# Kernel optimization log

Hardware: AMD Instinct MI355X
Metric: run time of the kernel (lower is better)

## Reference

```python
import jax, jax.numpy as jnp
import numpy as np

K = 20
NEG = jnp.float32(-1e30)

def _l2norm(x):
    # F.normalize(x, dim=1, p=2) with eps clamp
    n = jnp.sqrt(jnp.sum(x * x, axis=1, keepdims=True))
    return x / jnp.maximum(n, 1e-12)

def setup_inputs() -> dict:
    key = jax.random.key(0)
    k1, k2, k3 = jax.random.split(key, 3)
    h, w, C = 96, 96, 256
    query_label = jax.random.randint(k1, (h, w, 3), 0, 2, dtype=jnp.int64)
    color = jnp.zeros((3,), dtype=jnp.int64)
    q_feat = jax.random.normal(k2, (1, C, h, w), dtype=jnp.float32)
    s_feat = jax.random.normal(k3, (1, C, h, w), dtype=jnp.float32)
    return {"query_label": query_label, "color": color, "q_feat": q_feat, "s_feat": s_feat}

def reference(query_label, color, q_feat, s_feat):
    C = q_feat.shape[1]
    out_hw = s_feat.shape[2:]
    # mask at feature resolution (query_label already sized [h,w,3])
    mask = jnp.all(query_label == color, axis=-1).reshape(-1)      # [M]
    q = q_feat[0].transpose(1, 2, 0).reshape(-1, C)                # [M,C]
    s = s_feat[0].transpose(1, 2, 0).reshape(-1, C)                # [N,C]
    qn = _l2norm(q)
    sn = _l2norm(s)
    sim = sn @ qn.T                                                # [N,M] cosine sims
    # top-K over fg columns == top-K over full row with non-fg masked to -inf
    fg_top = jax.lax.top_k(jnp.where(mask[None, :], sim, NEG), K)[0]
    bg_top = jax.lax.top_k(jnp.where(mask[None, :], NEG, sim), K)[0]
    fg_score = jnp.mean(fg_top, axis=1).reshape(out_hw)
    bg_score = jnp.mean(bg_top, axis=1).reshape(out_hw)
    return fg_score, bg_score
```

## Files before the change

kernel.cpp:

```cpp
#include <hip/hip_runtime.h>
#include <math.h>

#define MTOT 9216
#define CDIM 256
#define KSEL 20
#define NCHUNK 4
#define CHUNKQ 2304
#define BS 32
#define QSTEP 128
#define NSTEP 18
#define NSLAB 72

typedef __attribute__((ext_vector_type(8))) short short8;
typedef __attribute__((ext_vector_type(8))) unsigned short ushort8;
typedef __attribute__((ext_vector_type(4))) float f32x4;
typedef __attribute__((ext_vector_type(2))) _Float16 h2;

__device__ __forceinline__ unsigned short f2bf(float v) {
    unsigned u = __float_as_uint(v);
    u += 0x7FFF + ((u >> 16) & 1);
    return (unsigned short)(u >> 16);
}
__device__ __forceinline__ h2 pkh2(float lo, float hi) {
    auto r = __builtin_amdgcn_cvt_pkrtz(lo, hi);
    h2 h; __builtin_memcpy(&h, &r, 4); return h;
}
__device__ __forceinline__ h2 asH2(unsigned int u) {
    h2 h; __builtin_memcpy(&h, &u, 4); return h;
}
__device__ __forceinline__ unsigned int h2u(h2 h) {
    unsigned int u; __builtin_memcpy(&u, &h, 4); return u;
}
__device__ __forceinline__ h2 h2max(h2 a, h2 b) {
    h2 d; asm("v_pk_max_f16 %0, %1, %2" : "=v"(d) : "v"(a), "v"(b)); return d;
}
__device__ __forceinline__ h2 h2min(h2 a, h2 b) {
    h2 d; asm("v_pk_min_f16 %0, %1, %2" : "=v"(d) : "v"(a), "v"(b)); return d;
}
__device__ __forceinline__ unsigned short hbits(_Float16 x) {
    unsigned short u; __builtin_memcpy(&u, &x, 2); return u;
}
__device__ __forceinline__ float hs2f(unsigned short u) {
    _Float16 x; __builtin_memcpy(&x, &u, 2); return (float)x;
}

__device__ __forceinline__ void ins20p(h2 (&l)[KSEL], h2 v) {
    v = h2max(v, l[0]);
#pragma unroll
    for (int i = 0; i < KSEL - 1; ++i) {
        h2 nxt = l[i + 1];
        l[i] = h2min(nxt, v);
        v = h2max(nxt, v);
    }
    l[KSEL - 1] = v;
}
__device__ __forceinline__ void ins20(float (&l)[KSEL], float v) {
#pragma unroll
    for (int i = 0; i < KSEL - 1; ++i) {
        float nxt = l[i + 1];
        l[i] = fminf(nxt, v);
        v = fmaxf(nxt, v);
    }
    l[KSEL - 1] = v;
}

__global__ __launch_bounds__(256) void prepconv_kernel(
    const int* __restrict__ ql, const int* __restrict__ color,
    const float* __restrict__ qf, const float* __restrict__ sf,
    int* __restrict__ cnt,
    unsigned short* __restrict__ qbt, unsigned short* __restrict__ sbt)
{
    __shared__ float tilef[32 * 257];
    __shared__ float red[256];
    __shared__ float invv[32];
    __shared__ int slotl[32];
    const int bid = blockIdx.x;
    const bool isQ = bid < (MTOT / 32);
    const int m0 = (isQ ? bid : bid - MTOT / 32) * 32;
    const float* src = isQ ? qf : sf;
    const int t = threadIdx.x;
    const int ml = t & 31, cb = t >> 5;
    float sq = 0.f;
#pragma unroll
    for (int i = 0; i < 32; ++i) {
        int c = cb * 32 + i;
        float v = src[c * MTOT + m0 + ml];
        tilef[ml * 257 + c] = v;
        sq += v * v;
    }
    red[cb * 32 + ml] = sq;
    __syncthreads();
    if (t < 32) {
        float s = 0.f;
#pragma unroll
        for (int j = 0; j < 8; ++j) s += red[j * 32 + t];
        invv[t] = 1.0f / fmaxf(sqrtf(s), 1e-12f);
        if (isQ) {
            int m = m0 + t;
            bool fg = (ql[3*m] == color[0]) & (ql[3*m+1] == color[1]) & (ql[3*m+2] == color[2]);
            slotl[t] = fg ? atomicAdd(&cnt[0], 1) : (MTOT - 1 - atomicAdd(&cnt[1], 1));
        }
    }
    __syncthreads();
    const int row = t >> 3, seg = t & 7;
    const float iv = invv[row];
    const int drow = isQ ? slotl[row] : (m0 + row);
    unsigned short* dst = (isQ ? qbt : sbt) + (size_t)drow * 256 + seg * 32;
    const float* srcr = &tilef[row * 257 + seg * 32];
#pragma unroll
    for (int ch = 0; ch < 4; ++ch) {
        ushort8 o;
#pragma unroll
        for (int e = 0; e < 8; ++e) o[e] = f2bf(srcr[ch * 8 + e] * iv);
        *(ushort8*)(dst + ch * 8) = o;
    }
}

__global__ __launch_bounds__(256, 3) void matchsim_kernel(
    const unsigned short* __restrict__ qbt, const unsigned short* __restrict__ sbt,
    const int* __restrict__ cnt, unsigned short* __restrict__ part)
{
    __shared__ __align__(16) char smem[49152];
    unsigned int* mbuf = (unsigned int*)smem;

    const int t = threadIdx.x;
    const int w = t >> 6, l = t & 63;
    const int sblk = blockIdx.x >> 2;
    const int chunk = blockIdx.x & 3;
    const int s0 = sblk * BS;
    const int q0c = chunk * CHUNKQ;
    const int fgc = cnt[0];

    {
        int row = t >> 3, cb = t & 7;
        const ushort8* gs = (const ushort8*)(sbt + (size_t)(s0 + row) * 256);
#pragma unroll
        for (int i = 0; i < 4; ++i) {
            int ch = cb + i * 8;
            ushort8 v = gs[ch];
            int byte = (row * 512 + ch * 16) ^ ((row & 7) << 4);
            *(ushort8*)(smem + byte) = v;
        }
    }
    __syncthreads();

    const h2 NEG2 = { (_Float16)-65504.f, (_Float16)-65504.f };
    h2 fgl[KSEL], bgl[KSEL];
#pragma unroll
    for (int i = 0; i < KSEL; ++i) { fgl[i] = NEG2; bgl[i] = NEG2; }

    ushort8 qr[4];
    const int wl = (t & 63) >> 1;
    const int qhalf = t & 1;
    auto loadQ = [&](int gslab) {
        int step = gslab >> 2, slab = gslab & 3;
        const unsigned short* base =
            qbt + (size_t)(q0c + step * QSTEP + w * 32 + wl) * 256 + slab * 64 + qhalf * 32;
#pragma unroll
        for (int i = 0; i < 4; ++i)
            qr[i] = *(const ushort8*)(base + i * 8);
    };
    loadQ(0);
    const int qwswz = (wl & 7) << 4;
    char* const qbase = smem + 16384 + w * 4096;

    const int lg = l >> 4;
    const int aq0 = l & 15;
    const int aq1 = aq0 + 16;
    const int aswz0 = (aq0 & 7) << 4, aswz1 = (aq1 & 7) << 4;
    const int srow0 = l & 15, srow1 = srow0 + 16;
    const int bswz0 = (srow0 & 7) << 4, bswz1 = (srow1 & 7) << 4;

    f32x4 acc00 = {0,0,0,0}, acc01 = {0,0,0,0}, acc10 = {0,0,0,0}, acc11 = {0,0,0,0};
    int cur = 0;

    for (int gslab = 0; gslab < NSLAB; ++gslab) {
        char* Qs = qbase + cur * 16384;
#pragma unroll
        for (int i = 0; i < 4; ++i) {
            int byte = (wl * 128 + qhalf * 64 + i * 16) ^ qwswz;
            *(ushort8*)(Qs + byte) = qr[i];
        }
        if (gslab + 1 < NSLAB) loadQ(gslab + 1);
        const int slab = gslab & 3;
        __builtin_amdgcn_s_setprio(1);
#pragma unroll
        for (int ks = 0; ks < 2; ++ks) {
            int ak = ks * 64 + lg * 16;
            short8 a0 = *(const short8*)(Qs + ((aq0 * 128 + ak) ^ aswz0));
            short8 a1 = *(const short8*)(Qs + ((aq1 * 128 + ak) ^ aswz1));
            int bk = slab * 128 + ks * 64 + lg * 16;
            short8 b0 = *(const short8*)(smem + ((srow0 * 512 + bk) ^ bswz0));
            short8 b1 = *(const short8*)(smem + ((srow1 * 512 + bk) ^ bswz1));
            acc00 = __builtin_amdgcn_mfma_f32_16x16x32_bf16(a0, b0, acc00, 0, 0, 0);
            acc01 = __builtin_amdgcn_mfma_f32_16x16x32_bf16(a0, b1, acc01, 0, 0, 0);
            acc10 = __builtin_amdgcn_mfma_f32_16x16x32_bf16(a1, b0, acc10, 0, 0, 0);
            acc11 = __builtin_amdgcn_mfma_f32_16x16x32_bf16(a1, b1, acc11, 0, 0, 0);
        }
        __builtin_amdgcn_s_setprio(0);
        cur ^= 1;
        if (slab == 3) {
            const int step = gslab >> 2;
            const int qw0 = q0c + step * QSTEP + w * 32;
#pragma unroll
            for (int qt = 0; qt < 2; ++qt) {
                const f32x4& aS0 = qt ? acc10 : acc00;
                const f32x4& aS1 = qt ? acc11 : acc01;
                int qfirst = qw0 + qt * 16;
                if (qfirst + 16 <= fgc) {
#pragma unroll
                    for (int r = 0; r < 4; ++r) ins20p(fgl, pkh2(aS0[r], aS1[r]));
                } else if (qfirst >= fgc) {
#pragma unroll
                    for (int r = 0; r < 4; ++r) ins20p(bgl, pkh2(aS0[r], aS1[r]));
                } else {
#pragma unroll
                    for (int r = 0; r < 4; ++r) {
                        h2 v = pkh2(aS0[r], aS1[r]);
                        bool m = (qfirst + lg * 4 + r) < fgc;
                        ins20p(fgl, m ? v : NEG2);
                        ins20p(bgl, m ? NEG2 : v);
                    }
                }
            }
            acc00 = (f32x4){0,0,0,0}; acc01 = (f32x4){0,0,0,0};
            acc10 = (f32x4){0,0,0,0}; acc11 = (f32x4){0,0,0,0};
        }
    }

    __syncthreads();
    const int sp = l & 15, owner = w * 4 + lg;
    auto midx = [](int cls, int own, int spi) { return ((cls * 16 + own) * 16 + spi) * 21; };
    {
        unsigned int* df = &mbuf[midx(0, owner, sp)];
        unsigned int* db = &mbuf[midx(1, owner, sp)];
#pragma unroll
        for (int k = 0; k < KSEL; ++k) { df[k] = h2u(fgl[k]); db[k] = h2u(bgl[k]); }
    }
    __syncthreads();
    auto mergeL = [&](unsigned int* A, const unsigned int* B) {
        h2 la[KSEL];
#pragma unroll
        for (int k = 0; k < KSEL; ++k) la[k] = asH2(A[k]);
        for (int j = KSEL - 1; j >= 0; --j) {
            h2 v = asH2(B[j]);
            if (!(v.x > la[0].x || v.y > la[0].y)) break;
            ins20p(la, v);
        }
#pragma unroll
        for (int k = 0; k < KSEL; ++k) A[k] = h2u(la[k]);
    };
    {
        int cls = t >> 7, u = t & 127, spi = u & 15, j = u >> 4;
        mergeL(&mbuf[midx(cls, j, spi)], &mbuf[midx(cls, j + 8, spi)]);
    }
    __syncthreads();
    if (t < 128) {
        int cls = t >> 6, u = t & 63, spi = u & 15, j = u >> 4;
        mergeL(&mbuf[midx(cls, j, spi)], &mbuf[midx(cls, j + 4, spi)]);
    }
    __syncthreads();
    if (t < 64) {
        int cls = t >> 5, u = t & 31, spi = u & 15, j = u >> 4;
        mergeL(&mbuf[midx(cls, j, spi)], &mbuf[midx(cls, j + 2, spi)]);
    }
    __syncthreads();
    if (t < 32) {
        int cls = t >> 4, spi = t & 15;
        unsigned int* A = &mbuf[midx(cls, 0, spi)];
        const unsigned int* B = &mbuf[midx(cls, 1, spi)];
        h2 la[KSEL];
#pragma unroll
        for (int k = 0; k < KSEL; ++k) la[k] = asH2(A[k]);
        for (int j = KSEL - 1; j >= 0; --j) {
            h2 v = asH2(B[j]);
            if (!(v.x > la[0].x || v.y > la[0].y)) break;
            ins20p(la, v);
        }
        unsigned short* d0 = &part[((size_t)(s0 + spi)      * NCHUNK + chunk) * (2*KSEL) + cls*KSEL];
        unsigned short* d1 = &part[((size_t)(s0 + 16 + spi) * NCHUNK + chunk) * (2*KSEL) + cls*KSEL];
#pragma unroll
        for (int k = 0; k < KSEL; ++k) {
            d0[k] = hbits(la[k].x);
            d1[k] = hbits(la[k].y);
        }
    }
}

__global__ __launch_bounds__(256) void finalize_kernel(
    const unsigned short* __restrict__ part, float* __restrict__ out)
{
    int n = blockIdx.x * 256 + threadIdx.x;
    if (n >= MTOT) return;
    const unsigned short* base = part + (size_t)n * NCHUNK * 2 * KSEL;
#pragma unroll
    for (int cls = 0; cls < 2; ++cls) {
        float la[KSEL];
        const unsigned short* c0p = base + cls * KSEL;
#pragma unroll
        for (int k = 0; k < KSEL; ++k) la[k] = hs2f(c0p[k]);
        for (int ch = 1; ch < NCHUNK; ++ch) {
            const unsigned short* sp = base + ch * 2 * KSEL + cls * KSEL;
            for (int j = KSEL - 1; j >= 0; --j) {
                float v = hs2f(sp[j]);
                if (v <= la[0]) break;
                ins20(la, v);
            }
        }
        float s = 0.f;
#pragma unroll
        for (int k = 0; k < KSEL; ++k) s += la[k];
        out[cls * MTOT + n] = s * (1.0f / KSEL);
    }
}

extern "C" void kernel_launch(void* const* d_in, const int* in_sizes, int n_in,
                              void* d_out, int out_size, void* d_ws, size_t ws_size,
                              hipStream_t stream) {
    const int*   ql    = (const int*)d_in[0];
    const int*   color = (const int*)d_in[1];
    const float* qf    = (const float*)d_in[2];
    const float* sf    = (const float*)d_in[3];
    float* out = (float*)d_out;

    int* cnt = (int*)d_ws;
    unsigned short* qbt = (unsigned short*)(cnt + 4);
    unsigned short* sbt = qbt + (size_t)MTOT * CDIM;
    unsigned short* part = sbt + (size_t)MTOT * CDIM;

    (void)hipMemsetAsync(cnt, 0, 16, stream);
    prepconv_kernel<<<2 * (MTOT / 32), 256, 0, stream>>>(ql, color, qf, sf, cnt, qbt, sbt);
    matchsim_kernel<<<(MTOT / BS) * NCHUNK, 256, 0, stream>>>(qbt, sbt, cnt, part);
    finalize_kernel<<<MTOT / 256, 256, 0, stream>>>(part, out);
}
```

Baseline: 183.1 us.

## Cache support B fragments in registers and split query range into eight chunks

```diff
diff --git a/kernel.cpp b/kernel.cpp
--- a/kernel.cpp
+++ b/kernel.cpp
@@ -4,12 +4,12 @@
 #define MTOT 9216
 #define CDIM 256
 #define KSEL 20
-#define NCHUNK 4
-#define CHUNKQ 2304
+#define NCHUNK 8
+#define CHUNKQ 1152
 #define BS 32
 #define QSTEP 128
-#define NSTEP 18
-#define NSLAB 72
+#define NSTEP 9
+#define NSLAB 36
 
 typedef __attribute__((ext_vector_type(8))) short short8;
 typedef __attribute__((ext_vector_type(8))) unsigned short ushort8;
@@ -125,8 +125,8 @@
 
     const int t = threadIdx.x;
     const int w = t >> 6, l = t & 63;
-    const int sblk = blockIdx.x >> 2;
-    const int chunk = blockIdx.x & 3;
+    const int sblk = blockIdx.x >> 3;
+    const int chunk = blockIdx.x & 7;
     const int s0 = sblk * BS;
     const int q0c = chunk * CHUNKQ;
     const int fgc = cnt[0];
@@ -144,14 +144,31 @@
     }
     __syncthreads();
 
+    const int lg = l >> 4;
+    const int aq0 = l & 15;
+    const int aq1 = aq0 + 16;
+    const int aswz0 = (aq0 & 7) << 4, aswz1 = (aq1 & 7) << 4;
+    const int srow0 = l & 15, srow1 = srow0 + 16;
+    const int bswz0 = (srow0 & 7) << 4, bswz1 = (srow1 & 7) << 4;
+
+    short8 Bf[16];
+#pragma unroll
+    for (int sl = 0; sl < 4; ++sl)
+#pragma unroll
+        for (int ks = 0; ks < 2; ++ks) {
+            int bk = sl * 128 + ks * 64 + lg * 16;
+            Bf[sl * 4 + ks * 2 + 0] = *(const short8*)(smem + ((srow0 * 512 + bk) ^ bswz0));
+            Bf[sl * 4 + ks * 2 + 1] = *(const short8*)(smem + ((srow1 * 512 + bk) ^ bswz1));
+        }
+
     const h2 NEG2 = { (_Float16)-65504.f, (_Float16)-65504.f };
     h2 fgl[KSEL], bgl[KSEL];
 #pragma unroll
     for (int i = 0; i < KSEL; ++i) { fgl[i] = NEG2; bgl[i] = NEG2; }
 
-    ushort8 qr[4];
     const int wl = (t & 63) >> 1;
     const int qhalf = t & 1;
+    ushort8 qr[4];
     auto loadQ = [&](int gslab) {
         int step = gslab >> 2, slab = gslab & 3;
         const unsigned short* base =
@@ -164,68 +181,56 @@
     const int qwswz = (wl & 7) << 4;
     char* const qbase = smem + 16384 + w * 4096;
 
-    const int lg = l >> 4;
-    const int aq0 = l & 15;
-    const int aq1 = aq0 + 16;
-    const int aswz0 = (aq0 & 7) << 4, aswz1 = (aq1 & 7) << 4;
-    const int srow0 = l & 15, srow1 = srow0 + 16;
-    const int bswz0 = (srow0 & 7) << 4, bswz1 = (srow1 & 7) << 4;
-
     f32x4 acc00 = {0,0,0,0}, acc01 = {0,0,0,0}, acc10 = {0,0,0,0}, acc11 = {0,0,0,0};
-    int cur = 0;
-
-    for (int gslab = 0; gslab < NSLAB; ++gslab) {
-        char* Qs = qbase + cur * 16384;
-#pragma unroll
-        for (int i = 0; i < 4; ++i) {
-            int byte = (wl * 128 + qhalf * 64 + i * 16) ^ qwswz;
-            *(ushort8*)(Qs + byte) = qr[i];
-        }
-        if (gslab + 1 < NSLAB) loadQ(gslab + 1);
-        const int slab = gslab & 3;
-        __builtin_amdgcn_s_setprio(1);
-#pragma unroll
-        for (int ks = 0; ks < 2; ++ks) {
-            int ak = ks * 64 + lg * 16;
-            short8 a0 = *(const short8*)(Qs + ((aq0 * 128 + ak) ^ aswz0));
-            short8 a1 = *(const short8*)(Qs + ((aq1 * 128 + ak) ^ aswz1));
-            int bk = slab * 128 + ks * 64 + lg * 16;
-            short8 b0 = *(const short8*)(smem + ((srow0 * 512 + bk) ^ bswz0));
-            short8 b1 = *(const short8*)(smem + ((srow1 * 512 + bk) ^ bswz1));
-            acc00 = __builtin_amdgcn_mfma_f32_16x16x32_bf16(a0, b0, acc00, 0, 0, 0);
-            acc01 = __builtin_amdgcn_mfma_f32_16x16x32_bf16(a0, b1, acc01, 0, 0, 0);
-            acc10 = __builtin_amdgcn_mfma_f32_16x16x32_bf16(a1, b0, acc10, 0, 0, 0);
-            acc11 = __builtin_amdgcn_mfma_f32_16x16x32_bf16(a1, b1, acc11, 0, 0, 0);
-        }
-        __builtin_amdgcn_s_setprio(0);
-        cur ^= 1;
-        if (slab == 3) {
-            const int step = gslab >> 2;
-            const int qw0 = q0c + step * QSTEP + w * 32;
-#pragma unroll
-            for (int qt = 0; qt < 2; ++qt) {
-                const f32x4& aS0 = qt ? acc10 : acc00;
-                const f32x4& aS1 = qt ? acc11 : acc01;
-                int qfirst = qw0 + qt * 16;
-                if (qfirst + 16 <= fgc) {
-#pragma unroll
-                    for (int r = 0; r < 4; ++r) ins20p(fgl, pkh2(aS0[r], aS1[r]));
-                } else if (qfirst >= fgc) {
-#pragma unroll
-                    for (int r = 0; r < 4; ++r) ins20p(bgl, pkh2(aS0[r], aS1[r]));
-                } else {
-#pragma unroll
-                    for (int r = 0; r < 4; ++r) {
-                        h2 v = pkh2(aS0[r], aS1[r]);
-                        bool m = (qfirst + lg * 4 + r) < fgc;
-                        ins20p(fgl, m ? v : NEG2);
-                        ins20p(bgl, m ? NEG2 : v);
-                    }
+
+    for (int step = 0; step < NSTEP; ++step) {
+#pragma unroll
+        for (int sl = 0; sl < 4; ++sl) {
+            const int gslab = step * 4 + sl;
+            char* Qs = qbase + (sl & 1) * 16384;
+#pragma unroll
+            for (int i = 0; i < 4; ++i) {
+                int byte = (wl * 128 + qhalf * 64 + i * 16) ^ qwswz;
+                *(ushort8*)(Qs + byte) = qr[i];
+            }
+            if (gslab + 1 < NSLAB) loadQ(gslab + 1);
+            __builtin_amdgcn_s_setprio(1);
+#pragma unroll
+            for (int ks = 0; ks < 2; ++ks) {
+                int ak = ks * 64 + lg * 16;
+                short8 a0 = *(const short8*)(Qs + ((aq0 * 128 + ak) ^ aswz0));
+                short8 a1 = *(const short8*)(Qs + ((aq1 * 128 + ak) ^ aswz1));
+                acc00 = __builtin_amdgcn_mfma_f32_16x16x32_bf16(a0, Bf[sl*4+ks*2+0], acc00, 0, 0, 0);
+                acc01 = __builtin_amdgcn_mfma_f32_16x16x32_bf16(a0, Bf[sl*4+ks*2+1], acc01, 0, 0, 0);
+                acc10 = __builtin_amdgcn_mfma_f32_16x16x32_bf16(a1, Bf[sl*4+ks*2+0], acc10, 0, 0, 0);
+                acc11 = __builtin_amdgcn_mfma_f32_16x16x32_bf16(a1, Bf[sl*4+ks*2+1], acc11, 0, 0, 0);
+            }
+            __builtin_amdgcn_s_setprio(0);
+        }
+        const int qw0 = q0c + step * QSTEP + w * 32;
+#pragma unroll
+        for (int qt = 0; qt < 2; ++qt) {
+            const f32x4& aS0 = qt ? acc10 : acc00;
+            const f32x4& aS1 = qt ? acc11 : acc01;
+            int qfirst = qw0 + qt * 16;
+            if (qfirst + 16 <= fgc) {
+#pragma unroll
+                for (int r = 0; r < 4; ++r) ins20p(fgl, pkh2(aS0[r], aS1[r]));
+            } else if (qfirst >= fgc) {
+#pragma unroll
+                for (int r = 0; r < 4; ++r) ins20p(bgl, pkh2(aS0[r], aS1[r]));
+            } else {
+#pragma unroll
+                for (int r = 0; r < 4; ++r) {
+                    h2 v = pkh2(aS0[r], aS1[r]);
+                    bool m = (qfirst + lg * 4 + r) < fgc;
+                    ins20p(fgl, m ? v : NEG2);
+                    ins20p(bgl, m ? NEG2 : v);
                 }
             }
-            acc00 = (f32x4){0,0,0,0}; acc01 = (f32x4){0,0,0,0};
-            acc10 = (f32x4){0,0,0,0}; acc11 = (f32x4){0,0,0,0};
-        }
+        }
+        acc00 = (f32x4){0,0,0,0}; acc01 = (f32x4){0,0,0,0};
+        acc10 = (f32x4){0,0,0,0}; acc11 = (f32x4){0,0,0,0};
     }
 
     __syncthreads();
```

Result: slower. 238.5 us (+30.2%).
